# Kernel tuning notes

Measured on AMD Instinct MI355X. Metric: run time of the kernel, lower is better.

Reference implementation:

```python
import jax, jax.numpy as jnp
import numpy as np
from jax import lax

# bior3.5 decomposition low-pass filter (pywt.Wavelet('bior3.5').dec_lo)
_BIOR35_DEC_LO = [-0.013810679320049757, 0.04143203796014927, 0.052480581416189075,
                  -0.26792717880896527, -0.07181553246425873, 0.966747552403483,
                  0.966747552403483, -0.07181553246425873, -0.26792717880896527,
                  0.052480581416189075, 0.04143203796014927, -0.013810679320049757]

J = 3  # decomposition levels


def setup_inputs() -> dict:
    key = jax.random.key(0)
    x = jax.random.normal(key, (16, 64, 16384), dtype=jnp.float32)
    hac = jnp.asarray(np.array(_BIOR35_DEC_LO, dtype=np.float32))
    return {"x": x, "hac": hac}


def _afb1d(x, h0, h1):
    """Analysis filter bank: stride-2 depthwise conv over last dim.

    x: (B, C, N); h0, h1: (L,). Returns (lo, hi), each (B, C, outsize).
    Since every channel uses the same pair of filters, we fold (B, C) into
    the batch dim and run a single-input-channel, 2-output-channel conv.
    """
    B, C, N = x.shape
    L = h0.shape[0]
    outsize = (N + L - 1) // 2              # pywt 'zero' mode coeff length
    p = 2 * (outsize - 1) - N + L           # total padding needed
    if p % 2 == 1:                          # odd -> extra zero on the right
        x = jnp.pad(x, ((0, 0), (0, 0), (0, 1)))
        N += 1
        p -= 1
    half = p // 2
    xr = x.reshape(B * C, 1, N)
    k = jnp.stack([h0, h1])[:, None, :]     # (2, 1, L) -- cross-correlation, like torch
    out = lax.conv_general_dilated(xr, k, window_strides=(2,),
                                   padding=[(half, half)],
                                   dimension_numbers=('NCH', 'OIH', 'NCH'))
    lo = out[:, 0, :].reshape(B, C, outsize)
    hi = out[:, 1, :].reshape(B, C, outsize)
    return lo, hi


def reference(x, hac):
    L = hac.shape[0]
    # QMF pair: h1[i] = (-1)^(i+1) * h0[L-1-i]  (miu[::2] = -1 in torch code)
    sign = jnp.where(jnp.arange(L) % 2 == 0, -1.0, 1.0).astype(hac.dtype)
    h0 = hac
    h1 = hac[::-1] * sign
    x0 = x
    highs = []
    for _ in range(J):
        x0, x1 = _afb1d(x0, h0, h1)
        highs.append(x1)
    return (x0, *highs)
```

## Files before the change

kernel.cpp:

```cpp
#include <hip/hip_runtime.h>


#define FILT_LEN 12
#define ROWS  1024
#define N1    16384
#define O1    8197
#define O2    4104
#define O3    2057
#define NBLK  4
#define T1    2050
#define T2    1026
#define T3    515
#define NTHR  256

#define XCAP   4288
#define L1CAP  2112
#define LO2_OFF  2112
#define HB2_OFF  3200
#define LO3_OFF  0
#define HI3_OFF  544

constexpr int cmin(int a, int b) { return a < b ? a : b; }
constexpr int cmax(int a, int b) { return a > b ? a : b; }

__device__ __forceinline__ int sw4(int f4) { return f4 ^ ((f4 >> 3) & 7); }
__device__ __forceinline__ float4 ld4(const float* p, int f4) {
    return reinterpret_cast<const float4*>(p)[sw4(f4)];
}
__device__ __forceinline__ void st4(float* p, int f4, float4 v) {
    reinterpret_cast<float4*>(p)[sw4(f4)] = v;
}
__device__ __forceinline__ float ldss(const float* p, int j) {
    return p[(sw4(j >> 2) << 2) | (j & 3)];
}
__device__ __forceinline__ void stss(float* p, int j, float v) {
    p[(sw4(j >> 2) << 2) | (j & 3)] = v;
}

__device__ __forceinline__ float h0tap(int i) {
    constexpr float H[FILT_LEN] = {
        -0.013810679320049757f, 0.04143203796014927f, 0.052480581416189075f,
        -0.26792717880896527f, -0.07181553246425873f, 0.966747552403483f,
        0.966747552403483f, -0.07181553246425873f, -0.26792717880896527f,
        0.052480581416189075f, 0.04143203796014927f, -0.013810679320049757f};
    return H[i];
}

template<int B>
struct Cfg {
    static constexpr int s1 = B * T1, e1 = cmin(s1 + T1, O1);
    static constexpr int s2 = B * T2, e2 = cmin(s2 + T2, O2);
    static constexpr int s3 = B * T3, e3 = cmin(s3 + T3, O3);
    static constexpr int c2s = cmax(0, cmin(s2, 2 * s3 - 10));
    static constexpr int c2e = cmin(O2, cmax(e2, 2 * e3));
    static constexpr int c1s = cmax(0, cmin(s1, 2 * c2s - 10)) & ~1;
    static constexpr int c1e = cmin(O1, cmax(e1, 2 * c2e));
    static constexpr int span1 = c1e - c1s;
    static constexpr int span2 = c2e - c2s;
    static constexpr int span3 = e3 - s3;
    static constexpr int xbase = 2 * c1s - 12;
    static constexpr int D2 = 2 * c2s - 10 - c1s + 12;
    static constexpr int ab2 = D2 & ~3, p2 = D2 & 3;
    static constexpr int D3 = 2 * s3 - 10 - c2s + 12;
    static constexpr int ab3 = D3 & ~3, p3 = D3 & 3;
    static constexpr int zt1 = 2104 - (12 + span1);
    static constexpr int zt2 = 1056 - (12 + span2);
};

template<int B>
__device__ __forceinline__ void body(
    const float* __restrict__ xrow,
    float* __restrict__ lo3r, float* __restrict__ hi1r,
    float* __restrict__ hi2r, float* __restrict__ hi3r,
    float* __restrict__ xs, float* __restrict__ l1, const int tid)
{
    using C = Cfg<B>;

    float h0[FILT_LEN], h1[FILT_LEN];
#pragma unroll
    for (int i = 0; i < FILT_LEN; ++i) {
        h0[i] = h0tap(i);
        h1[i] = h0tap(FILT_LEN - 1 - i) * ((i & 1) ? 1.0f : -1.0f);
    }

    if constexpr (C::xbase >= 0 && C::xbase + XCAP <= N1) {
        for (int i = tid; i < XCAP / 4; i += NTHR)
            st4(xs, i, *reinterpret_cast<const float4*>(xrow + C::xbase + 4 * i));
    } else {
        for (int i = tid; i < XCAP / 4; i += NTHR) {
            const int g0 = C::xbase + 4 * i;
            float4 v;
            if (g0 >= 0 && g0 + 4 <= N1) {
                v = *reinterpret_cast<const float4*>(xrow + g0);
            } else {
                v.x = ((unsigned)(g0 + 0) < (unsigned)N1) ? xrow[g0 + 0] : 0.f;
                v.y = ((unsigned)(g0 + 1) < (unsigned)N1) ? xrow[g0 + 1] : 0.f;
                v.z = ((unsigned)(g0 + 2) < (unsigned)N1) ? xrow[g0 + 2] : 0.f;
                v.w = ((unsigned)(g0 + 3) < (unsigned)N1) ? xrow[g0 + 3] : 0.f;
            }
            st4(xs, i, v);
        }
    }
    if (tid < 12)      stss(l1, tid, 0.f);
    if (tid < C::zt1)  stss(l1, 12 + C::span1 + tid, 0.f);
    __syncthreads();

    float hr1[2][8];
#pragma unroll
    for (int r = 0; r < 2; ++r) {
        const int tt0 = tid * 8 + r * 2048;
        if (tt0 < C::span1) {
            float w[28];
            const int f0 = tid * 4 + r * 1024;
#pragma unroll
            for (int m = 0; m < 7; ++m) {
                const float4 v = ld4(xs, f0 + m);
                w[4 * m + 0] = v.x; w[4 * m + 1] = v.y;
                w[4 * m + 2] = v.z; w[4 * m + 3] = v.w;
            }
            float a0[8], a1[8];
#pragma unroll
            for (int k = 0; k < 8; ++k) { a0[k] = 0.f; a1[k] = 0.f; }
#pragma unroll
            for (int l = 0; l < FILT_LEN; ++l) {
#pragma unroll
                for (int k = 0; k < 8; ++k) {
                    const float v = w[2 * k + 2 + l];
                    a0[k] = fmaf(v, h0[l], a0[k]);
                    a1[k] = fmaf(v, h1[l], a1[k]);
                }
            }
            if (tt0 + 8 <= C::span1) {
                st4(l1, 3 + tid * 2 + r * 512,
                    make_float4(a0[0], a0[1], a0[2], a0[3]));
                st4(l1, 4 + tid * 2 + r * 512,
                    make_float4(a0[4], a0[5], a0[6], a0[7]));
            } else {
#pragma unroll
                for (int k = 0; k < 8; ++k)
                    if (tt0 + k < C::span1) stss(l1, 12 + tt0 + k, a0[k]);
            }
#pragma unroll
            for (int k = 0; k < 8; ++k) hr1[r][k] = a1[k];
        }
    }
    __syncthreads();

#pragma unroll
    for (int r = 0; r < 2; ++r) {
        const int tt0 = tid * 8 + r * 2048;
        if (tt0 < C::span1) {
            if (tt0 + 8 <= C::span1) {
                st4(xs, tid * 2 + r * 512,
                    make_float4(hr1[r][0], hr1[r][1], hr1[r][2], hr1[r][3]));
                st4(xs, tid * 2 + r * 512 + 1,
                    make_float4(hr1[r][4], hr1[r][5], hr1[r][6], hr1[r][7]));
            } else {
#pragma unroll
                for (int k = 0; k < 8; ++k)
                    if (tt0 + k < C::span1) stss(xs, tt0 + k, hr1[r][k]);
            }
        }
    }
    if (tid < 12)      stss(xs, LO2_OFF + tid, 0.f);
    if (tid < C::zt2)  stss(xs, LO2_OFF + 12 + C::span2 + tid, 0.f);

    float hr2[2][4];
#pragma unroll
    for (int r = 0; r < 2; ++r) {
        const int tt0 = tid * 4 + r * 1024;
        if (tt0 < C::span2) {
            float w[20];
            const int f0 = tid * 2 + r * 512 + (C::ab2 >> 2);
#pragma unroll
            for (int m = 0; m < 5; ++m) {
                const float4 v = ld4(l1, f0 + m);
                w[4 * m + 0] = v.x; w[4 * m + 1] = v.y;
                w[4 * m + 2] = v.z; w[4 * m + 3] = v.w;
            }
            float a0[4], a1[4];
#pragma unroll
            for (int k = 0; k < 4; ++k) { a0[k] = 0.f; a1[k] = 0.f; }
#pragma unroll
            for (int l = 0; l < FILT_LEN; ++l) {
#pragma unroll
                for (int k = 0; k < 4; ++k) {
                    const float v = w[2 * k + l + C::p2];
                    a0[k] = fmaf(v, h0[l], a0[k]);
                    a1[k] = fmaf(v, h1[l], a1[k]);
                }
            }
            if (tt0 + 4 <= C::span2) {
                st4(xs, 531 + tid + r * 256,
                    make_float4(a0[0], a0[1], a0[2], a0[3]));
            } else {
#pragma unroll
                for (int k = 0; k < 4; ++k)
                    if (tt0 + k < C::span2) stss(xs, LO2_OFF + 12 + tt0 + k, a0[k]);
            }
#pragma unroll
            for (int k = 0; k < 4; ++k) hr2[r][k] = a1[k];
        }
    }
    __syncthreads();

    for (int i = (C::s1 - C::c1s) + tid; i < C::e1 - C::c1s; i += NTHR)
        hi1r[C::c1s + i] = ldss(xs, i);

#pragma unroll
    for (int r = 0; r < 2; ++r) {
        const int tt0 = tid * 4 + r * 1024;
        if (tt0 < C::span2) {
            if (tt0 + 4 <= C::span2) {
                st4(xs, (HB2_OFF >> 2) + tid + r * 256,
                    make_float4(hr2[r][0], hr2[r][1], hr2[r][2], hr2[r][3]));
            } else {
#pragma unroll
                for (int k = 0; k < 4; ++k)
                    if (tt0 + k < C::span2) stss(xs, HB2_OFF + tt0 + k, hr2[r][k]);
            }
        }
    }

#pragma unroll
    for (int r = 0; r < 2; ++r) {
        const int tt0 = tid * 2 + r * 512;
        if (tt0 < C::span3) {
            float w[16];
            const int f0 = (LO2_OFF >> 2) + tid + r * 256 + (C::ab3 >> 2);
#pragma unroll
            for (int m = 0; m < 4; ++m) {
                const float4 v = ld4(xs, f0 + m);
                w[4 * m + 0] = v.x; w[4 * m + 1] = v.y;
                w[4 * m + 2] = v.z; w[4 * m + 3] = v.w;
            }
            float a0[2], a1[2];
#pragma unroll
            for (int k = 0; k < 2; ++k) { a0[k] = 0.f; a1[k] = 0.f; }
#pragma unroll
            for (int l = 0; l < FILT_LEN; ++l) {
#pragma unroll
                for (int k = 0; k < 2; ++k) {
                    const float v = w[2 * k + l + C::p3];
                    a0[k] = fmaf(v, h0[l], a0[k]);
                    a1[k] = fmaf(v, h1[l], a1[k]);
                }
            }
#pragma unroll
            for (int k = 0; k < 2; ++k) {
                if (tt0 + k < C::span3) {
                    stss(l1, LO3_OFF + tt0 + k, a0[k]);
                    stss(l1, HI3_OFF + tt0 + k, a1[k]);
                }
            }
        }
    }
    __syncthreads();

    for (int i = (C::s2 - C::c2s) + tid; i < C::e2 - C::c2s; i += NTHR)
        hi2r[C::c2s + i] = ldss(xs, HB2_OFF + i);
    for (int i = tid; i < C::span3; i += NTHR) {
        lo3r[C::s3 + i] = ldss(l1, LO3_OFF + i);
        hi3r[C::s3 + i] = ldss(l1, HI3_OFF + i);
    }
}

__global__ __launch_bounds__(NTHR, 6) void dwt_fused_kernel(
    const float* __restrict__ x,
    float* __restrict__ lo3, float* __restrict__ hi1,
    float* __restrict__ hi2, float* __restrict__ hi3)
{
    __shared__ __align__(16) float xs[XCAP];
    __shared__ __align__(16) float l1[L1CAP];

    const int row = blockIdx.y;
    const int tid = threadIdx.x;
    const float* xrow = x + (size_t)row * N1;
    float* lo3r = lo3 + (size_t)row * O3;
    float* hi1r = hi1 + (size_t)row * O1;
    float* hi2r = hi2 + (size_t)row * O2;
    float* hi3r = hi3 + (size_t)row * O3;

    switch (blockIdx.x) {
        case 0:  body<0>(xrow, lo3r, hi1r, hi2r, hi3r, xs, l1, tid); break;
        case 1:  body<1>(xrow, lo3r, hi1r, hi2r, hi3r, xs, l1, tid); break;
        case 2:  body<2>(xrow, lo3r, hi1r, hi2r, hi3r, xs, l1, tid); break;
        default: body<3>(xrow, lo3r, hi1r, hi2r, hi3r, xs, l1, tid); break;
    }
}

extern "C" void kernel_launch(void* const* d_in, const int* in_sizes, int n_in,
                              void* d_out, int out_size, void* d_ws, size_t ws_size,
                              hipStream_t stream)
{
    const float* x = (const float*)d_in[0];
    float* out = (float*)d_out;

    float* lo3 = out;
    float* hi1 = out + (size_t)ROWS * O3;
    float* hi2 = hi1 + (size_t)ROWS * O1;
    float* hi3 = hi2 + (size_t)ROWS * O2;

    dwt_fused_kernel<<<dim3(NBLK, ROWS), dim3(NTHR), 0, stream>>>(
        x, lo3, hi1, hi2, hi3);
}
```

Before: 120.2 us.

## Split each row into eight tiles and restructure fused 3-level DWT passes

Each row now splits across 8 blocks instead of 4, so every thread handles a single 8-output pass per level. The shared-memory buffers are resized, and level-2 lo/hi results are written straight to shared memory instead of being held in registers across a barrier. The hi1/hi2 stores are moved ahead of the level-3 compute, which removes one __syncthreads. Filter taps become constexpr immediates, launch bounds are raised to 8 blocks per SIMD, and static_asserts check the layout. More blocks raise occupancy and parallelism, at the cost of more redundant halo loads and recomputation at tile boundaries.

```diff
diff --git a/kernel.cpp b/kernel.cpp
--- a/kernel.cpp
+++ b/kernel.cpp
@@ -7,18 +7,18 @@
 #define O1    8197
 #define O2    4104
 #define O3    2057
-#define NBLK  4
-#define T1    2050
-#define T2    1026
-#define T3    515
+#define NBLK  8
+#define T1    1025
+#define T2    513
+#define T3    258
 #define NTHR  256
 
-#define XCAP   4288
-#define L1CAP  2112
-#define LO2_OFF  2112
-#define HB2_OFF  3200
-#define LO3_OFF  0
-#define HI3_OFF  544
+#define XCAP    2208
+#define L1CAP   1120
+#define LO2_OFF 1088
+#define LO2SZ   560
+#define HB2_OFF 1664
+#define HI3_OFF 272
 
 constexpr int cmin(int a, int b) { return a < b ? a : b; }
 constexpr int cmax(int a, int b) { return a > b ? a : b; }
@@ -37,7 +37,7 @@
     p[(sw4(j >> 2) << 2) | (j & 3)] = v;
 }
 
-__device__ __forceinline__ float h0tap(int i) {
+__device__ __forceinline__ constexpr float h0tap(int i) {
     constexpr float H[FILT_LEN] = {
         -0.013810679320049757f, 0.04143203796014927f, 0.052480581416189075f,
         -0.26792717880896527f, -0.07181553246425873f, 0.966747552403483f,
@@ -45,13 +45,16 @@
         0.052480581416189075f, 0.04143203796014927f, -0.013810679320049757f};
     return H[i];
 }
+__device__ __forceinline__ constexpr float h1tap(int i) {
+    return h0tap(FILT_LEN - 1 - i) * ((i & 1) ? 1.0f : -1.0f);
+}
 
 template<int B>
 struct Cfg {
     static constexpr int s1 = B * T1, e1 = cmin(s1 + T1, O1);
     static constexpr int s2 = B * T2, e2 = cmin(s2 + T2, O2);
     static constexpr int s3 = B * T3, e3 = cmin(s3 + T3, O3);
-    static constexpr int c2s = cmax(0, cmin(s2, 2 * s3 - 10));
+    static constexpr int c2s = cmax(0, cmin(s2, 2 * s3 - 10)) & ~1;
     static constexpr int c2e = cmin(O2, cmax(e2, 2 * e3));
     static constexpr int c1s = cmax(0, cmin(s1, 2 * c2s - 10)) & ~1;
     static constexpr int c1e = cmin(O1, cmax(e1, 2 * c2e));
@@ -63,8 +66,26 @@
     static constexpr int ab2 = D2 & ~3, p2 = D2 & 3;
     static constexpr int D3 = 2 * s3 - 10 - c2s + 12;
     static constexpr int ab3 = D3 & ~3, p3 = D3 & 3;
-    static constexpr int zt1 = 2104 - (12 + span1);
-    static constexpr int zt2 = 1056 - (12 + span2);
+    static constexpr int zt1 = L1CAP - (12 + span1);
+    static constexpr int zt2 = LO2SZ - (12 + span2);
+    static constexpr int o1s = s1 - c1s, o1e = e1 - c1s;
+    static constexpr int o2s = s2 - c2s, o2e = e2 - c2s;
+
+    static_assert(D2 >= 0 && D3 >= 0, "pad origin");
+    static_assert((D2 & 1) == 0 && (D3 & 1) == 0, "window parity (R5 bug)");
+    static_assert(p2 <= 2 && p3 <= 2, "window shift fits 28-float window");
+    static_assert((xbase & 3) == 0, "x staging alignment");
+    static_assert(zt1 >= 0 && zt1 <= NTHR, "l1 tail zero in one pass");
+    static_assert(zt2 >= 0 && zt2 <= NTHR, "lo2 tail zero in one pass");
+    static_assert(span1 <= 8 * NTHR && span2 <= 8 * NTHR && span3 <= 8 * NTHR,
+                  "single K=8 pass");
+    static_assert(2 * (((span1 - 1) / 8) * 8) + 25 + 2 < XCAP, "L1 window read");
+    static_assert(2 * (((span2 - 1) / 8) * 8) + ab2 + 25 + p2 < L1CAP, "L2 window read");
+    static_assert(2 * (((span3 - 1) / 8) * 8) + ab3 + 25 + p3 < LO2SZ, "L3 window read");
+    static_assert(span1 <= LO2_OFF, "hi1 stash fits");
+    static_assert(HB2_OFF + span2 <= XCAP, "hi2 stash fits");
+    static_assert(HI3_OFF + span3 <= L1CAP, "hi3 stash fits");
+    static_assert(HI3_OFF >= span3, "lo3/hi3 disjoint");
 };
 
 template<int B>
@@ -76,16 +97,11 @@
 {
     using C = Cfg<B>;
 
-    float h0[FILT_LEN], h1[FILT_LEN];
-#pragma unroll
-    for (int i = 0; i < FILT_LEN; ++i) {
-        h0[i] = h0tap(i);
-        h1[i] = h0tap(FILT_LEN - 1 - i) * ((i & 1) ? 1.0f : -1.0f);
-    }
-
     if constexpr (C::xbase >= 0 && C::xbase + XCAP <= N1) {
-        for (int i = tid; i < XCAP / 4; i += NTHR)
-            st4(xs, i, *reinterpret_cast<const float4*>(xrow + C::xbase + 4 * i));
+        st4(xs, tid,       *reinterpret_cast<const float4*>(xrow + C::xbase + 4 * tid));
+        st4(xs, tid + 256, *reinterpret_cast<const float4*>(xrow + C::xbase + 1024 + 4 * tid));
+        if (tid < XCAP / 4 - 512)
+            st4(xs, tid + 512, *reinterpret_cast<const float4*>(xrow + C::xbase + 2048 + 4 * tid));
     } else {
         for (int i = tid; i < XCAP / 4; i += NTHR) {
             const int g0 = C::xbase + 4 * i;
@@ -105,16 +121,59 @@
     if (tid < C::zt1)  stss(l1, 12 + C::span1 + tid, 0.f);
     __syncthreads();
 
-    float hr1[2][8];
-#pragma unroll
-    for (int r = 0; r < 2; ++r) {
-        const int tt0 = tid * 8 + r * 2048;
-        if (tt0 < C::span1) {
+    float hr1[8];
+    const int tt1 = tid * 8;
+    if (tt1 < C::span1) {
+        float w[28];
+#pragma unroll
+        for (int m = 0; m < 7; ++m) {
+            const float4 v = ld4(xs, tid * 4 + m);
+            w[4 * m + 0] = v.x; w[4 * m + 1] = v.y;
+            w[4 * m + 2] = v.z; w[4 * m + 3] = v.w;
+        }
+        float a0[8];
+#pragma unroll
+        for (int k = 0; k < 8; ++k) { a0[k] = 0.f; hr1[k] = 0.f; }
+#pragma unroll
+        for (int l = 0; l < FILT_LEN; ++l) {
+#pragma unroll
+            for (int k = 0; k < 8; ++k) {
+                const float v = w[2 * k + 2 + l];
+                a0[k]  = fmaf(v, h0tap(l), a0[k]);
+                hr1[k] = fmaf(v, h1tap(l), hr1[k]);
+            }
+        }
+        if (tt1 + 8 <= C::span1) {
+            st4(l1, 3 + 2 * tid, make_float4(a0[0], a0[1], a0[2], a0[3]));
+            st4(l1, 4 + 2 * tid, make_float4(a0[4], a0[5], a0[6], a0[7]));
+        } else {
+#pragma unroll
+            for (int k = 0; k < 8; ++k)
+                if (tt1 + k < C::span1) stss(l1, 12 + tt1 + k, a0[k]);
+        }
+    }
+    __syncthreads();
+
+    if (tt1 < C::span1) {
+        if (tt1 + 8 <= C::span1) {
+            st4(xs, 2 * tid,     make_float4(hr1[0], hr1[1], hr1[2], hr1[3]));
+            st4(xs, 2 * tid + 1, make_float4(hr1[4], hr1[5], hr1[6], hr1[7]));
+        } else {
+#pragma unroll
+            for (int k = 0; k < 8; ++k)
+                if (tt1 + k < C::span1) stss(xs, tt1 + k, hr1[k]);
+        }
+    }
+    if (tid < 12)      stss(xs, LO2_OFF + tid, 0.f);
+    if (tid < C::zt2)  stss(xs, LO2_OFF + 12 + C::span2 + tid, 0.f);
+
+    {
+        const int tt2 = tid * 8;
+        if (tt2 < C::span2) {
             float w[28];
-            const int f0 = tid * 4 + r * 1024;
 #pragma unroll
             for (int m = 0; m < 7; ++m) {
-                const float4 v = ld4(xs, f0 + m);
+                const float4 v = ld4(l1, tid * 4 + (C::ab2 >> 2) + m);
                 w[4 * m + 0] = v.x; w[4 * m + 1] = v.y;
                 w[4 * m + 2] = v.z; w[4 * m + 3] = v.w;
             }
@@ -125,147 +184,81 @@
             for (int l = 0; l < FILT_LEN; ++l) {
 #pragma unroll
                 for (int k = 0; k < 8; ++k) {
-                    const float v = w[2 * k + 2 + l];
-                    a0[k] = fmaf(v, h0[l], a0[k]);
-                    a1[k] = fmaf(v, h1[l], a1[k]);
+                    const float v = w[2 * k + l + C::p2];
+                    a0[k] = fmaf(v, h0tap(l), a0[k]);
+                    a1[k] = fmaf(v, h1tap(l), a1[k]);
                 }
             }
-            if (tt0 + 8 <= C::span1) {
-                st4(l1, 3 + tid * 2 + r * 512,
-                    make_float4(a0[0], a0[1], a0[2], a0[3]));
-                st4(l1, 4 + tid * 2 + r * 512,
-                    make_float4(a0[4], a0[5], a0[6], a0[7]));
+            if (tt2 + 8 <= C::span2) {
+                st4(xs, 275 + 2 * tid, make_float4(a0[0], a0[1], a0[2], a0[3]));
+                st4(xs, 276 + 2 * tid, make_float4(a0[4], a0[5], a0[6], a0[7]));
+                st4(xs, 416 + 2 * tid, make_float4(a1[0], a1[1], a1[2], a1[3]));
+                st4(xs, 417 + 2 * tid, make_float4(a1[4], a1[5], a1[6], a1[7]));
             } else {
 #pragma unroll
-                for (int k = 0; k < 8; ++k)
-                    if (tt0 + k < C::span1) stss(l1, 12 + tt0 + k, a0[k]);
-            }
-#pragma unroll
-            for (int k = 0; k < 8; ++k) hr1[r][k] = a1[k];
+                for (int k = 0; k < 8; ++k) {
+                    if (tt2 + k < C::span2) {
+                        stss(xs, LO2_OFF + 12 + tt2 + k, a0[k]);
+                        stss(xs, HB2_OFF + tt2 + k, a1[k]);
+                    }
+                }
+            }
         }
     }
     __syncthreads();
 
-#pragma unroll
-    for (int r = 0; r < 2; ++r) {
-        const int tt0 = tid * 8 + r * 2048;
-        if (tt0 < C::span1) {
-            if (tt0 + 8 <= C::span1) {
-                st4(xs, tid * 2 + r * 512,
-                    make_float4(hr1[r][0], hr1[r][1], hr1[r][2], hr1[r][3]));
-                st4(xs, tid * 2 + r * 512 + 1,
-                    make_float4(hr1[r][4], hr1[r][5], hr1[r][6], hr1[r][7]));
-            } else {
-#pragma unroll
-                for (int k = 0; k < 8; ++k)
-                    if (tt0 + k < C::span1) stss(xs, tt0 + k, hr1[r][k]);
-            }
-        }
-    }
-    if (tid < 12)      stss(xs, LO2_OFF + tid, 0.f);
-    if (tid < C::zt2)  stss(xs, LO2_OFF + 12 + C::span2 + tid, 0.f);
-
-    float hr2[2][4];
-#pragma unroll
-    for (int r = 0; r < 2; ++r) {
-        const int tt0 = tid * 4 + r * 1024;
-        if (tt0 < C::span2) {
-            float w[20];
-            const int f0 = tid * 2 + r * 512 + (C::ab2 >> 2);
-#pragma unroll
-            for (int m = 0; m < 5; ++m) {
-                const float4 v = ld4(l1, f0 + m);
+    for (int i = C::o1s + tid; i < C::o1e; i += NTHR)
+        hi1r[C::c1s + i] = ldss(xs, i);
+    for (int i = C::o2s + tid; i < C::o2e; i += NTHR)
+        hi2r[C::c2s + i] = ldss(xs, HB2_OFF + i);
+
+    {
+        const int tt3 = tid * 8;
+        if (tt3 < C::span3) {
+            float w[28];
+#pragma unroll
+            for (int m = 0; m < 7; ++m) {
+                const float4 v = ld4(xs, (LO2_OFF >> 2) + tid * 4 + (C::ab3 >> 2) + m);
                 w[4 * m + 0] = v.x; w[4 * m + 1] = v.y;
                 w[4 * m + 2] = v.z; w[4 * m + 3] = v.w;
             }
-            float a0[4], a1[4];
-#pragma unroll
-            for (int k = 0; k < 4; ++k) { a0[k] = 0.f; a1[k] = 0.f; }
+            float a0[8], a1[8];
+#pragma unroll
+            for (int k = 0; k < 8; ++k) { a0[k] = 0.f; a1[k] = 0.f; }
 #pragma unroll
             for (int l = 0; l < FILT_LEN; ++l) {
 #pragma unroll
-                for (int k = 0; k < 4; ++k) {
-                    const float v = w[2 * k + l + C::p2];
-                    a0[k] = fmaf(v, h0[l], a0[k]);
-                    a1[k] = fmaf(v, h1[l], a1[k]);
+                for (int k = 0; k < 8; ++k) {
+                    const float v = w[2 * k + l + C::p3];
+                    a0[k] = fmaf(v, h0tap(l), a0[k]);
+                    a1[k] = fmaf(v, h1tap(l), a1[k]);
                 }
             }
-            if (tt0 + 4 <= C::span2) {
-                st4(xs, 531 + tid + r * 256,
-                    make_float4(a0[0], a0[1], a0[2], a0[3]));
+            if (tt3 + 8 <= C::span3) {
+                st4(l1, 2 * tid,                     make_float4(a0[0], a0[1], a0[2], a0[3]));
+                st4(l1, 2 * tid + 1,                 make_float4(a0[4], a0[5], a0[6], a0[7]));
+                st4(l1, (HI3_OFF >> 2) + 2 * tid,     make_float4(a1[0], a1[1], a1[2], a1[3]));
+                st4(l1, (HI3_OFF >> 2) + 2 * tid + 1, make_float4(a1[4], a1[5], a1[6], a1[7]));
             } else {
 #pragma unroll
-                for (int k = 0; k < 4; ++k)
-                    if (tt0 + k < C::span2) stss(xs, LO2_OFF + 12 + tt0 + k, a0[k]);
-            }
-#pragma unroll
-            for (int k = 0; k < 4; ++k) hr2[r][k] = a1[k];
+                for (int k = 0; k < 8; ++k) {
+                    if (tt3 + k < C::span3) {
+                        stss(l1, tt3 + k, a0[k]);
+                        stss(l1, HI3_OFF + tt3 + k, a1[k]);
+                    }
+                }
+            }
         }
     }
     __syncthreads();
 
-    for (int i = (C::s1 - C::c1s) + tid; i < C::e1 - C::c1s; i += NTHR)
-        hi1r[C::c1s + i] = ldss(xs, i);
-
-#pragma unroll
-    for (int r = 0; r < 2; ++r) {
-        const int tt0 = tid * 4 + r * 1024;
-        if (tt0 < C::span2) {
-            if (tt0 + 4 <= C::span2) {
-                st4(xs, (HB2_OFF >> 2) + tid + r * 256,
-                    make_float4(hr2[r][0], hr2[r][1], hr2[r][2], hr2[r][3]));
-            } else {
-#pragma unroll
-                for (int k = 0; k < 4; ++k)
-                    if (tt0 + k < C::span2) stss(xs, HB2_OFF + tt0 + k, hr2[r][k]);
-            }
-        }
-    }
-
-#pragma unroll
-    for (int r = 0; r < 2; ++r) {
-        const int tt0 = tid * 2 + r * 512;
-        if (tt0 < C::span3) {
-            float w[16];
-            const int f0 = (LO2_OFF >> 2) + tid + r * 256 + (C::ab3 >> 2);
-#pragma unroll
-            for (int m = 0; m < 4; ++m) {
-                const float4 v = ld4(xs, f0 + m);
-                w[4 * m + 0] = v.x; w[4 * m + 1] = v.y;
-                w[4 * m + 2] = v.z; w[4 * m + 3] = v.w;
-            }
-            float a0[2], a1[2];
-#pragma unroll
-            for (int k = 0; k < 2; ++k) { a0[k] = 0.f; a1[k] = 0.f; }
-#pragma unroll
-            for (int l = 0; l < FILT_LEN; ++l) {
-#pragma unroll
-                for (int k = 0; k < 2; ++k) {
-                    const float v = w[2 * k + l + C::p3];
-                    a0[k] = fmaf(v, h0[l], a0[k]);
-                    a1[k] = fmaf(v, h1[l], a1[k]);
-                }
-            }
-#pragma unroll
-            for (int k = 0; k < 2; ++k) {
-                if (tt0 + k < C::span3) {
-                    stss(l1, LO3_OFF + tt0 + k, a0[k]);
-                    stss(l1, HI3_OFF + tt0 + k, a1[k]);
-                }
-            }
-        }
-    }
-    __syncthreads();
-
-    for (int i = (C::s2 - C::c2s) + tid; i < C::e2 - C::c2s; i += NTHR)
-        hi2r[C::c2s + i] = ldss(xs, HB2_OFF + i);
     for (int i = tid; i < C::span3; i += NTHR) {
-        lo3r[C::s3 + i] = ldss(l1, LO3_OFF + i);
+        lo3r[C::s3 + i] = ldss(l1, i);
         hi3r[C::s3 + i] = ldss(l1, HI3_OFF + i);
     }
 }
 
-__global__ __launch_bounds__(NTHR, 6) void dwt_fused_kernel(
+__global__ __launch_bounds__(NTHR, 8) void dwt_fused_kernel(
     const float* __restrict__ x,
     float* __restrict__ lo3, float* __restrict__ hi1,
     float* __restrict__ hi2, float* __restrict__ hi3)
@@ -285,7 +278,11 @@
         case 0:  body<0>(xrow, lo3r, hi1r, hi2r, hi3r, xs, l1, tid); break;
         case 1:  body<1>(xrow, lo3r, hi1r, hi2r, hi3r, xs, l1, tid); break;
         case 2:  body<2>(xrow, lo3r, hi1r, hi2r, hi3r, xs, l1, tid); break;
-        default: body<3>(xrow, lo3r, hi1r, hi2r, hi3r, xs, l1, tid); break;
+        case 3:  body<3>(xrow, lo3r, hi1r, hi2r, hi3r, xs, l1, tid); break;
+        case 4:  body<4>(xrow, lo3r, hi1r, hi2r, hi3r, xs, l1, tid); break;
+        case 5:  body<5>(xrow, lo3r, hi1r, hi2r, hi3r, xs, l1, tid); break;
+        case 6:  body<6>(xrow, lo3r, hi1r, hi2r, hi3r, xs, l1, tid); break;
+        default: body<7>(xrow, lo3r, hi1r, hi2r, hi3r, xs, l1, tid); break;
     }
 }
 
```

Measured after the change: 118.8 us. About the same (-1.1%).
